# Optimization experiments

Hardware: AMD Instinct MI355X
Metric: run time of the kernel (lower is better)

## Reference

```python
import jax, jax.numpy as jnp
import numpy as np

B, N, E = 8, 5000, 40000
F, FE, FILTERS = 64, 16, 96
LN_EPS = 1e-3  # keras LayerNormalization default epsilon


def _layer_norm(x, gamma, beta):
    mu = jnp.mean(x, axis=-1, keepdims=True)
    var = jnp.mean(jnp.square(x - mu), axis=-1, keepdims=True)
    return (x - mu) * jax.lax.rsqrt(var + LN_EPS) * gamma + beta


def setup_inputs() -> dict:
    key = jax.random.key(0)
    ks = jax.random.split(key, 8)
    nodes = jax.random.normal(ks[0], (B, N, F), dtype=jnp.float32)
    edge_features = jax.random.normal(ks[1], (B, E, FE), dtype=jnp.float32)
    edges = jax.random.randint(ks[2], (B, E, 2), 0, N, dtype=jnp.int32)
    d_msg_in = 2 * F + FE   # 144
    d_upd_in = F + FILTERS  # 160
    Wm = jax.random.normal(ks[3], (d_msg_in, FILTERS), dtype=jnp.float32) / np.sqrt(d_msg_in)
    bm = jnp.zeros((FILTERS,), dtype=jnp.float32)
    Wu = jax.random.normal(ks[4], (d_upd_in, FILTERS), dtype=jnp.float32) / np.sqrt(d_upd_in)
    bu = jnp.zeros((FILTERS,), dtype=jnp.float32)
    ln_m_gamma = jnp.ones((FILTERS,), dtype=jnp.float32)
    ln_m_beta = jnp.zeros((FILTERS,), dtype=jnp.float32)
    ln_u_gamma = jnp.ones((FILTERS,), dtype=jnp.float32)
    ln_u_beta = jnp.zeros((FILTERS,), dtype=jnp.float32)
    return {"nodes": nodes, "edge_features": edge_features, "edges": edges,
            "Wm": Wm, "bm": bm, "ln_m_gamma": ln_m_gamma, "ln_m_beta": ln_m_beta,
            "Wu": Wu, "bu": bu, "ln_u_gamma": ln_u_gamma, "ln_u_beta": ln_u_beta}


def reference(nodes, edge_features, edges, Wm, bm, ln_m_gamma, ln_m_beta,
              Wu, bu, ln_u_gamma, ln_u_beta):
    b, n, f = nodes.shape
    e = edges.shape[1]
    # gather endpoint features: (B,E,2,F) -> (B,E,2F)   [tf.gather batch_dims=1 + reshape]
    gathered = jax.vmap(lambda nd, ed: nd[ed])(nodes, edges)
    messages_in = gathered.reshape(b, e, 2 * f)
    msg_in = jnp.concatenate([messages_in, edge_features], axis=-1)
    # message layer: Dense -> relu -> LayerNorm
    messages = jax.nn.relu(jnp.einsum('bec,cd->bed', msg_in, Wm) + bm)
    messages = _layer_norm(messages, ln_m_gamma, ln_m_beta)
    # aggregate: per-batch unsorted_segment_sum over destination node edges[...,1]
    aggregated = jax.vmap(
        lambda m, dst: jax.ops.segment_sum(m, dst, num_segments=n)
    )(messages, edges[..., 1])
    # update layer on [nodes, aggregated]: Dense -> relu -> LayerNorm
    upd_in = jnp.concatenate([nodes, aggregated], axis=-1)
    updated = jax.nn.relu(jnp.einsum('bnc,cd->bnd', upd_in, Wu) + bu)
    updated_nodes = _layer_norm(updated, ln_u_gamma, ln_u_beta)
    return updated_nodes, messages
```

## Files before the change

### kernel.cpp

```cpp
#include <hip/hip_runtime.h>
#include <hip/hip_bf16.h>

typedef short s16x8 __attribute__((ext_vector_type(8)));
typedef float f32x4 __attribute__((ext_vector_type(4)));

namespace {
constexpr int kB   = 8;
constexpr int kN   = 5000;
constexpr int kE   = 40000;
constexpr int kF   = 64;
constexpr int kFE  = 16;
constexpr int kFil = 96;
constexpr float kEps = 1e-3f;
constexpr int kBN = kB * kN;
constexpr int kBE = kB * kE;
constexpr int kKp = 160;
constexpr int kLd = 168;
constexpr int kBM = 128;
}

__device__ inline unsigned short f2bf(float x) {
    unsigned u = __float_as_uint(x);
    u += 0x7FFFu + ((u >> 16) & 1u);
    return (unsigned short)(u >> 16);
}

__device__ inline s16x8 pack8(const float4& a, const float4& b) {
    union { s16x8 s; __hip_bfloat162 h[4]; } r;
    r.h[0] = __float22bfloat162_rn(make_float2(a.x, a.y));
    r.h[1] = __float22bfloat162_rn(make_float2(a.z, a.w));
    r.h[2] = __float22bfloat162_rn(make_float2(b.x, b.y));
    r.h[3] = __float22bfloat162_rn(make_float2(b.z, b.w));
    return r.s;
}

__device__ inline s16x8 loadA8(const float* __restrict__ p) {
    const float4* q = reinterpret_cast<const float4*>(p);
    return pack8(q[0], q[1]);
}

__device__ inline void atomicPkAddBf16(short* addr, float lo, float hi) {
    __hip_bfloat162 v = __float22bfloat162_rn(make_float2(lo, hi));
    unsigned data;
    __builtin_memcpy(&data, &v, 4);
    asm volatile("global_atomic_pk_add_bf16 %0, %1, off"
                 :: "v"((unsigned long long)addr), "v"(data) : "memory");
}

__global__ void prep_wT(const float* __restrict__ Wm, const float* __restrict__ Wu,
                        short* __restrict__ wmT, short* __restrict__ wuT) {
    const int t = blockIdx.x * 256 + threadIdx.x;
    if (t >= 96 * kKp) return;
    const int n = t / kKp, k = t % kKp;
    wmT[t] = (k < 144) ? (short)f2bf(Wm[(size_t)k * 96 + n]) : (short)0;
    wuT[t] = (short)f2bf(Wu[(size_t)k * 96 + n]);
}

__device__ inline void gemm_ln_store(const s16x8 a[5], const short* sB,
                                     const float* __restrict__ bias,
                                     const float* __restrict__ gamma_,
                                     const float* __restrict__ beta_,
                                     float* __restrict__ out,
                                     const int* __restrict__ edges2,
                                     short* __restrict__ aggOut,
                                     int rowBase, int rowMax) {
    const int tid  = threadIdx.x;
    const int w    = tid >> 6;
    const int lane = tid & 63;
    const int cl   = lane & 15;
    const int quad = lane >> 4;

    f32x4 acc[6] = {};
#pragma unroll
    for (int ks = 0; ks < 5; ++ks) {
#pragma unroll
        for (int t = 0; t < 6; ++t) {
            s16x8 b = *reinterpret_cast<const s16x8*>(
                sB + (16 * t + cl) * kLd + ks * 32 + quad * 8);
            acc[t] = __builtin_amdgcn_mfma_f32_16x16x32_bf16(a[ks], b, acc[t], 0, 0, 0);
        }
    }

    float bmv[6], gv[6], bv[6];
#pragma unroll
    for (int t = 0; t < 6; ++t) {
        const int c = 16 * t + cl;
        bmv[t] = bias[c]; gv[t] = gamma_[c]; bv[t] = beta_[c];
    }
#pragma unroll
    for (int j = 0; j < 4; ++j) {
        float v0[6];
        float s = 0.f;
#pragma unroll
        for (int t = 0; t < 6; ++t) {
            v0[t] = fmaxf(acc[t][j] + bmv[t], 0.f);
            s += v0[t];
        }
        s += __shfl_xor(s, 1); s += __shfl_xor(s, 2);
        s += __shfl_xor(s, 4); s += __shfl_xor(s, 8);
        const float mu = s * (1.f / 96.f);
        float q = 0.f;
#pragma unroll
        for (int t = 0; t < 6; ++t) {
            const float d = v0[t] - mu;
            q = fmaf(d, d, q);
        }
        q += __shfl_xor(q, 1); q += __shfl_xor(q, 2);
        q += __shfl_xor(q, 4); q += __shfl_xor(q, 8);
        const float inv = rsqrtf(q * (1.f / 96.f) + kEps);
        const int row = rowBase + 16 * w + 4 * quad + j;
        if (row < rowMax) {
            float ov[6];
#pragma unroll
            for (int t = 0; t < 6; ++t)
                ov[t] = (v0[t] - mu) * inv * gv[t] + bv[t];
            float* orow = out + (size_t)row * kFil;
#pragma unroll
            for (int t = 0; t < 6; ++t)
                orow[16 * t + cl] = ov[t];
            if (aggOut) {
                const int ob = row / kE;
                const int dn = edges2[(size_t)row * 2 + 1];
                short* arow = aggOut + ((size_t)ob * kN + dn) * kFil;
#pragma unroll
                for (int t = 0; t < 6; ++t) {
                    const float other = __shfl_xor(ov[t], 1);
                    if ((cl & 1) == 0)
                        atomicPkAddBf16(arow + 16 * t + cl, ov[t], other);
                }
            }
        }
    }
}

__global__ __launch_bounds__(512, 4) void msg_mfma(
    const float* __restrict__ nodes, const float* __restrict__ efeat,
    const int* __restrict__ edges, const short* __restrict__ wmT,
    const float* __restrict__ bm, const float* __restrict__ g,
    const float* __restrict__ be, float* __restrict__ out_msg,
    short* __restrict__ agg) {
    __shared__ short sB[96 * kLd];
    const int tid  = threadIdx.x;
    const int w    = tid >> 6;
    const int lane = tid & 63;
    const int cl   = lane & 15;
    const int quad = lane >> 4;

    const int row = blockIdx.x * kBM + 16 * w + cl;
    const int b   = row / kE;
    const int2 e2 = reinterpret_cast<const int2*>(edges)[row];
    const float* srcp = nodes + ((size_t)b * kN + e2.x) * kF + 8 * quad;
    const float* dstp = nodes + ((size_t)b * kN + e2.y) * kF + 8 * quad;

    s16x8 a[5];
    a[0] = loadA8(srcp);
    a[1] = loadA8(srcp + 32);
    a[2] = loadA8(dstp);
    a[3] = loadA8(dstp + 32);
    if (quad < 2) {
        a[4] = loadA8(efeat + (size_t)row * kFE + 8 * quad);
    } else {
        s16x8 z = {};
        a[4] = z;
    }

    for (int i = tid; i < 96 * kKp / 8; i += 512) {
        const int n = i / 20, c = i % 20;
        *reinterpret_cast<s16x8*>(sB + n * kLd + 8 * c) =
            *reinterpret_cast<const s16x8*>(wmT + n * kKp + 8 * c);
    }
    __syncthreads();
    gemm_ln_store(a, sB, bm, g, be, out_msg, edges, agg,
                  blockIdx.x * kBM, kBE);
}

__global__ __launch_bounds__(512, 4) void upd_mfma(
    const float* __restrict__ nodes, const short* __restrict__ agg,
    const short* __restrict__ wuT, const float* __restrict__ bu,
    const float* __restrict__ g, const float* __restrict__ be,
    float* __restrict__ out_upd) {
    __shared__ short sB[96 * kLd];
    const int tid  = threadIdx.x;
    const int w    = tid >> 6;
    const int lane = tid & 63;
    const int cl   = lane & 15;
    const int quad = lane >> 4;

    const int node0 = blockIdx.x * kBM + 16 * w + cl;
    const int node  = (node0 < kBN) ? node0 : (kBN - 1);
    const float* np = nodes + (size_t)node * kF + 8 * quad;
    const short* ap = agg + (size_t)node * kFil;

    s16x8 a[5];
    a[0] = loadA8(np);
    a[1] = loadA8(np + 32);
    a[2] = *reinterpret_cast<const s16x8*>(ap + 8 * quad);
    a[3] = *reinterpret_cast<const s16x8*>(ap + 32 + 8 * quad);
    a[4] = *reinterpret_cast<const s16x8*>(ap + 64 + 8 * quad);

    for (int i = tid; i < 96 * kKp / 8; i += 512) {
        const int n = i / 20, c = i % 20;
        *reinterpret_cast<s16x8*>(sB + n * kLd + 8 * c) =
            *reinterpret_cast<const s16x8*>(wuT + n * kKp + 8 * c);
    }
    __syncthreads();
    gemm_ln_store(a, sB, bu, g, be, out_upd, nullptr, nullptr,
                  blockIdx.x * kBM, kBN);
}

extern "C" void kernel_launch(void* const* d_in, const int* in_sizes, int n_in,
                              void* d_out, int out_size, void* d_ws, size_t ws_size,
                              hipStream_t stream) {
    const float* nodes  = (const float*)d_in[0];
    const float* efeat  = (const float*)d_in[1];
    const int*   edges  = (const int*)d_in[2];
    const float* Wm     = (const float*)d_in[3];
    const float* bm     = (const float*)d_in[4];
    const float* ln_m_g = (const float*)d_in[5];
    const float* ln_m_b = (const float*)d_in[6];
    const float* Wu     = (const float*)d_in[7];
    const float* bu     = (const float*)d_in[8];
    const float* ln_u_g = (const float*)d_in[9];
    const float* ln_u_b = (const float*)d_in[10];

    float* out_upd = (float*)d_out;
    float* out_msg = (float*)d_out + (size_t)kBN * kFil;

    short* wmT = (short*)d_ws;
    short* wuT = wmT + 96 * kKp;
    short* agg = wuT + 96 * kKp;

    hipMemsetAsync(agg, 0, (size_t)kBN * kFil * sizeof(short), stream);
    prep_wT<<<(96 * kKp + 255) / 256, 256, 0, stream>>>(Wm, Wu, wmT, wuT);

    msg_mfma<<<kBE / kBM, 512, 0, stream>>>(
        nodes, efeat, edges, wmT, bm, ln_m_g, ln_m_b, out_msg, agg);
    upd_mfma<<<(kBN + kBM - 1) / kBM, 512, 0, stream>>>(
        nodes, agg, wuT, bu, ln_u_g, ln_u_b, out_upd);
}
```

Baseline: 292.4 us.

## Stage message rows in LDS to issue row-contiguous bf16 atomics and paired stores

```diff
diff --git a/kernel.cpp b/kernel.cpp
--- a/kernel.cpp
+++ b/kernel.cpp
@@ -15,8 +15,9 @@
 constexpr int kBN = kB * kN;
 constexpr int kBE = kB * kE;
 constexpr int kKp = 160;
-constexpr int kLd = 168;
+constexpr int kLd = 184;
 constexpr int kBM = 128;
+constexpr int kTS = 49;
 }
 
 __device__ inline unsigned short f2bf(float x) {
@@ -39,14 +40,6 @@
     return pack8(q[0], q[1]);
 }
 
-__device__ inline void atomicPkAddBf16(short* addr, float lo, float hi) {
-    __hip_bfloat162 v = __float22bfloat162_rn(make_float2(lo, hi));
-    unsigned data;
-    __builtin_memcpy(&data, &v, 4);
-    asm volatile("global_atomic_pk_add_bf16 %0, %1, off"
-                 :: "v"((unsigned long long)addr), "v"(data) : "memory");
-}
-
 __global__ void prep_wT(const float* __restrict__ Wm, const float* __restrict__ Wu,
                         short* __restrict__ wmT, short* __restrict__ wuT) {
     const int t = blockIdx.x * 256 + threadIdx.x;
@@ -63,6 +56,7 @@
                                      float* __restrict__ out,
                                      const int* __restrict__ edges2,
                                      short* __restrict__ aggOut,
+                                     unsigned* __restrict__ sTw,
                                      int rowBase, int rowMax) {
     const int tid  = threadIdx.x;
     const int w    = tid >> 6;
@@ -116,19 +110,36 @@
                 ov[t] = (v0[t] - mu) * inv * gv[t] + bv[t];
             float* orow = out + (size_t)row * kFil;
 #pragma unroll
-            for (int t = 0; t < 6; ++t)
-                orow[16 * t + cl] = ov[t];
-            if (aggOut) {
-                const int ob = row / kE;
-                const int dn = edges2[(size_t)row * 2 + 1];
-                short* arow = aggOut + ((size_t)ob * kN + dn) * kFil;
-#pragma unroll
-                for (int t = 0; t < 6; ++t) {
-                    const float other = __shfl_xor(ov[t], 1);
-                    if ((cl & 1) == 0)
-                        atomicPkAddBf16(arow + 16 * t + cl, ov[t], other);
+            for (int t = 0; t < 6; ++t) {
+                const float other = __shfl_xor(ov[t], 1);
+                if ((cl & 1) == 0) {
+                    float2 st; st.x = ov[t]; st.y = other;
+                    *reinterpret_cast<float2*>(orow + 16 * t + cl) = st;
+                    if (aggOut) {
+                        __hip_bfloat162 hv =
+                            __float22bfloat162_rn(make_float2(ov[t], other));
+                        unsigned dw;
+                        __builtin_memcpy(&dw, &hv, 4);
+                        sTw[(4 * quad + j) * kTS + 8 * t + (cl >> 1)] = dw;
+                    }
                 }
             }
+        }
+    }
+
+    if (aggOut) {
+        const int r    = lane >> 2;
+        const int edge = rowBase + 16 * w + r;
+        const int ob   = edge / kE;
+        const int dn   = edges2[(size_t)edge * 2 + 1];
+        short* arow = aggOut + ((size_t)ob * kN + dn) * kFil;
+#pragma unroll
+        for (int i = 0; i < 12; ++i) {
+            const int p = (lane & 3) * 12 + i;
+            const unsigned dw = sTw[r * kTS + p];
+            asm volatile("global_atomic_pk_add_bf16 %0, %1, off"
+                         :: "v"((unsigned long long)(arow + 2 * p)), "v"(dw)
+                         : "memory");
         }
     }
 }
@@ -140,6 +151,7 @@
     const float* __restrict__ be, float* __restrict__ out_msg,
     short* __restrict__ agg) {
     __shared__ short sB[96 * kLd];
+    __shared__ unsigned sT[8][16 * kTS];
     const int tid  = threadIdx.x;
     const int w    = tid >> 6;
     const int lane = tid & 63;
@@ -170,7 +182,7 @@
             *reinterpret_cast<const s16x8*>(wmT + n * kKp + 8 * c);
     }
     __syncthreads();
-    gemm_ln_store(a, sB, bm, g, be, out_msg, edges, agg,
+    gemm_ln_store(a, sB, bm, g, be, out_msg, edges, agg, sT[w],
                   blockIdx.x * kBM, kBE);
 }
 
@@ -204,7 +216,7 @@
             *reinterpret_cast<const s16x8*>(wuT + n * kKp + 8 * c);
     }
     __syncthreads();
-    gemm_ln_store(a, sB, bu, g, be, out_upd, nullptr, nullptr,
+    gemm_ln_store(a, sB, bu, g, be, out_upd, nullptr, nullptr, nullptr,
                   blockIdx.x * kBM, kBN);
 }
 
```

New measurement: 793.1 us. 171% more time.

## Split segment-sum scatter out of message GEMM into separate atomic kernel

Applied to the files above, without the earlier changes.

```diff
diff --git a/kernel.cpp b/kernel.cpp
--- a/kernel.cpp
+++ b/kernel.cpp
@@ -39,14 +39,6 @@
     return pack8(q[0], q[1]);
 }
 
-__device__ inline void atomicPkAddBf16(short* addr, float lo, float hi) {
-    __hip_bfloat162 v = __float22bfloat162_rn(make_float2(lo, hi));
-    unsigned data;
-    __builtin_memcpy(&data, &v, 4);
-    asm volatile("global_atomic_pk_add_bf16 %0, %1, off"
-                 :: "v"((unsigned long long)addr), "v"(data) : "memory");
-}
-
 __global__ void prep_wT(const float* __restrict__ Wm, const float* __restrict__ Wu,
                         short* __restrict__ wmT, short* __restrict__ wuT) {
     const int t = blockIdx.x * 256 + threadIdx.x;
@@ -61,8 +53,6 @@
                                      const float* __restrict__ gamma_,
                                      const float* __restrict__ beta_,
                                      float* __restrict__ out,
-                                     const int* __restrict__ edges2,
-                                     short* __restrict__ aggOut,
                                      int rowBase, int rowMax) {
     const int tid  = threadIdx.x;
     const int w    = tid >> 6;
@@ -110,35 +100,19 @@
         const float inv = rsqrtf(q * (1.f / 96.f) + kEps);
         const int row = rowBase + 16 * w + 4 * quad + j;
         if (row < rowMax) {
-            float ov[6];
+            float* orow = out + (size_t)row * kFil;
 #pragma unroll
             for (int t = 0; t < 6; ++t)
-                ov[t] = (v0[t] - mu) * inv * gv[t] + bv[t];
-            float* orow = out + (size_t)row * kFil;
-#pragma unroll
-            for (int t = 0; t < 6; ++t)
-                orow[16 * t + cl] = ov[t];
-            if (aggOut) {
-                const int ob = row / kE;
-                const int dn = edges2[(size_t)row * 2 + 1];
-                short* arow = aggOut + ((size_t)ob * kN + dn) * kFil;
-#pragma unroll
-                for (int t = 0; t < 6; ++t) {
-                    const float other = __shfl_xor(ov[t], 1);
-                    if ((cl & 1) == 0)
-                        atomicPkAddBf16(arow + 16 * t + cl, ov[t], other);
-                }
-            }
-        }
-    }
-}
-
-__global__ __launch_bounds__(512, 4) void msg_mfma(
+                orow[16 * t + cl] = (v0[t] - mu) * inv * gv[t] + bv[t];
+        }
+    }
+}
+
+__global__ __launch_bounds__(512, 4) void msg_gemm(
     const float* __restrict__ nodes, const float* __restrict__ efeat,
     const int* __restrict__ edges, const short* __restrict__ wmT,
     const float* __restrict__ bm, const float* __restrict__ g,
-    const float* __restrict__ be, float* __restrict__ out_msg,
-    short* __restrict__ agg) {
+    const float* __restrict__ be, float* __restrict__ out_msg) {
     __shared__ short sB[96 * kLd];
     const int tid  = threadIdx.x;
     const int w    = tid >> 6;
@@ -170,8 +144,25 @@
             *reinterpret_cast<const s16x8*>(wmT + n * kKp + 8 * c);
     }
     __syncthreads();
-    gemm_ln_store(a, sB, bm, g, be, out_msg, edges, agg,
-                  blockIdx.x * kBM, kBE);
+    gemm_ln_store(a, sB, bm, g, be, out_msg, blockIdx.x * kBM, kBE);
+}
+
+__global__ __launch_bounds__(256) void scatter_pk(
+    const float* __restrict__ out_msg, const int* __restrict__ edges,
+    short* __restrict__ agg) {
+    const int idx  = blockIdx.x * 256 + threadIdx.x;
+    const int edge = idx / 48;
+    const int pair = idx - edge * 48;
+    const int b    = edge / kE;
+    const int dn   = edges[(size_t)edge * 2 + 1];
+    const float2 v = reinterpret_cast<const float2*>(
+        out_msg + (size_t)edge * kFil)[pair];
+    __hip_bfloat162 hv = __float22bfloat162_rn(make_float2(v.x, v.y));
+    unsigned dw;
+    __builtin_memcpy(&dw, &hv, 4);
+    short* addr = agg + ((size_t)b * kN + dn) * kFil + 2 * pair;
+    asm volatile("global_atomic_pk_add_bf16 %0, %1, off"
+                 :: "v"((unsigned long long)addr), "v"(dw) : "memory");
 }
 
 __global__ __launch_bounds__(512, 4) void upd_mfma(
@@ -204,8 +195,7 @@
             *reinterpret_cast<const s16x8*>(wuT + n * kKp + 8 * c);
     }
     __syncthreads();
-    gemm_ln_store(a, sB, bu, g, be, out_upd, nullptr, nullptr,
-                  blockIdx.x * kBM, kBN);
+    gemm_ln_store(a, sB, bu, g, be, out_upd, blockIdx.x * kBM, kBN);
 }
 
 extern "C" void kernel_launch(void* const* d_in, const int* in_sizes, int n_in,
@@ -233,8 +223,9 @@
     hipMemsetAsync(agg, 0, (size_t)kBN * kFil * sizeof(short), stream);
     prep_wT<<<(96 * kKp + 255) / 256, 256, 0, stream>>>(Wm, Wu, wmT, wuT);
 
-    msg_mfma<<<kBE / kBM, 512, 0, stream>>>(
-        nodes, efeat, edges, wmT, bm, ln_m_g, ln_m_b, out_msg, agg);
+    msg_gemm<<<kBE / kBM, 512, 0, stream>>>(
+        nodes, efeat, edges, wmT, bm, ln_m_g, ln_m_b, out_msg);
+    scatter_pk<<<kBE * 48 / 256, 256, 0, stream>>>(out_msg, edges, agg);
     upd_mfma<<<(kBN + kBM - 1) / kBM, 512, 0, stream>>>(
         nodes, agg, wuT, bu, ln_u_g, ln_u_b, out_upd);
 }
```

After: 276.0 us. -5.6%, faster.
